# Kernel optimization log

Hardware: AMD Instinct MI355X
Metric: run time of the kernel (lower is better)

Reference implementation:

```python
import jax, jax.numpy as jnp
import numpy as np

B, Hs, Ws, DIM = 1, 48, 48, 768
NUM_HEADS, HEAD_DIM = 12, 64
RANK, ALPHA = 4, 1.0
SCALING = ALPHA / RANK
SCALE = HEAD_DIM ** -0.5


def setup_inputs() -> dict:
    key = jax.random.key(0)
    ks = jax.random.split(key, 13)
    s = lambda k, shape, sc=0.02: jax.random.normal(k, shape, jnp.float32) * sc
    return dict(
        x=jax.random.normal(ks[0], (B, Hs, Ws, DIM), jnp.float32),
        qkv_w=s(ks[1], (3 * DIM, DIM)),
        qkv_b=s(ks[2], (3 * DIM,)),
        proj_w=s(ks[3], (DIM, DIM)),
        proj_b=s(ks[4], (DIM,)),
        rel_pos_h=s(ks[5], (2 * Hs - 1, HEAD_DIM)),
        rel_pos_w=s(ks[6], (2 * Ws - 1, HEAD_DIM)),
        lora_q_A=s(ks[7], (RANK, DIM)),
        lora_q_B=s(ks[8], (DIM, RANK)),
        lora_k_A=s(ks[9], (RANK, DIM)),
        lora_k_B=s(ks[10], (DIM, RANK)),
        lora_v_A=s(ks[11], (RANK, DIM)),
        lora_v_B=s(ks[12], (DIM, RANK)),
    )


def _get_rel_pos(size, rel_pos):
    # q_size == k_size -> relative index = i - j + (size - 1)
    coords = jnp.arange(size)
    idx = coords[:, None] - coords[None, :] + (size - 1)
    return rel_pos[idx]  # [size, size, head_dim]


def reference(x, qkv_w, qkv_b, proj_w, proj_b, rel_pos_h, rel_pos_w,
              lora_q_A, lora_q_B, lora_k_A, lora_k_B, lora_v_A, lora_v_B):
    Bn, Hq, Wq, dim = x.shape
    N = Hq * Wq
    x_flat = x.reshape(Bn, N, dim)
    # frozen base qkv: [B, N, 3, nh, hd] -> [3, B, nh, N, hd]
    qkv = (x_flat @ qkv_w.T + qkv_b).reshape(Bn, N, 3, NUM_HEADS, HEAD_DIM)
    qkv = jnp.transpose(qkv, (2, 0, 3, 1, 4))

    def lora(A, Bm):
        d = (x_flat @ A.T @ Bm.T) * SCALING  # [B, N, dim]
        return jnp.transpose(d.reshape(Bn, N, NUM_HEADS, HEAD_DIM), (0, 2, 1, 3))

    q = (qkv[0] + lora(lora_q_A, lora_q_B)).reshape(Bn * NUM_HEADS, N, HEAD_DIM)
    k = (qkv[1] + lora(lora_k_A, lora_k_B)).reshape(Bn * NUM_HEADS, N, HEAD_DIM)
    v = (qkv[2] + lora(lora_v_A, lora_v_B)).reshape(Bn * NUM_HEADS, N, HEAD_DIM)

    attn = (q * SCALE) @ jnp.swapaxes(k, -2, -1)  # [B*nh, N, N]

    # decomposed relative position bias
    Rh = _get_rel_pos(Hq, rel_pos_h)  # [H, H, hd]
    Rw = _get_rel_pos(Wq, rel_pos_w)  # [W, W, hd]
    r_q = q.reshape(Bn * NUM_HEADS, Hq, Wq, HEAD_DIM)
    rel_h = jnp.einsum("bhwc,hkc->bhwk", r_q, Rh)
    rel_w = jnp.einsum("bhwc,wkc->bhwk", r_q, Rw)
    attn = (attn.reshape(-1, Hq, Wq, Hq, Wq)
            + rel_h[:, :, :, :, None]
            + rel_w[:, :, :, None, :]).reshape(-1, N, N)

    attn = jax.nn.softmax(attn, axis=-1)
    out = (attn @ v).reshape(Bn, NUM_HEADS, Hq, Wq, HEAD_DIM)
    out = jnp.transpose(out, (0, 2, 3, 1, 4)).reshape(Bn, Hq, Wq, dim)
    return out @ proj_w.T + proj_b
```

## Files before the change

### kernel.cpp

```cpp
#include <hip/hip_runtime.h>

#define NTOK 2304
#define NH 12
#define HD 64

typedef __attribute__((ext_vector_type(8))) short bf16x8;
typedef __attribute__((ext_vector_type(4))) float f32x4;

__device__ __forceinline__ unsigned short f2bf(float f){
  union { float f; unsigned u; } v; v.f = f;
  unsigned r = v.u + 0x7fffu + ((v.u >> 16) & 1u);
  return (unsigned short)(r >> 16);
}
__device__ __forceinline__ float bf2f(unsigned short h){
  union { unsigned u; float f; } v; v.u = ((unsigned)h) << 16;
  return v.f;
}
__device__ __forceinline__ float fast_exp2(float x){
  float r;
  asm("v_exp_f32 %0, %1" : "=v"(r) : "v"(x));
  return r;
}
__device__ __forceinline__ void gload_lds16(const void* g, void* lds){
  __builtin_amdgcn_global_load_lds(
    (const __attribute__((address_space(1))) unsigned int*)g,
    (__attribute__((address_space(3))) unsigned int*)lds, 16, 0, 0);
}

__global__ __launch_bounds__(256) void cvt_all(
    const float* __restrict__ x, const float* __restrict__ qw, const float* __restrict__ pw,
    unsigned short* __restrict__ xb, unsigned short* __restrict__ wqb, unsigned short* __restrict__ wpb){
  int i = blockIdx.x * 256 + threadIdx.x;
  const float* src; unsigned short* dst; int off;
  if (i < 442368)      { src = x;  dst = xb;  off = i; }
  else if (i < 884736) { src = qw; dst = wqb; off = i - 442368; }
  else                 { src = pw; dst = wpb; off = i - 884736; }
  float4 v = ((const float4*)src)[off];
  union { unsigned short u[4]; unsigned long long ll; } o;
  o.u[0] = f2bf(v.x); o.u[1] = f2bf(v.y); o.u[2] = f2bf(v.z); o.u[3] = f2bf(v.w);
  ((unsigned long long*)dst)[off] = o.ll;
}

__global__ __launch_bounds__(256) void lora_t_kernel(const float* __restrict__ x,
    const float* __restrict__ Aq, const float* __restrict__ Ak, const float* __restrict__ Av,
    float* __restrict__ t){
  int wave = (blockIdx.x * 256 + threadIdx.x) >> 6;
  int lane = threadIdx.x & 63;
  if (wave >= NTOK) return;
  const float* xr = x + (size_t)wave * 768;
  float part[12];
  #pragma unroll
  for (int j = 0; j < 12; j++) part[j] = 0.f;
  for (int k = lane; k < 768; k += 64){
    float xv = xr[k];
    #pragma unroll
    for (int r = 0; r < 4; r++){
      part[r]     += xv * Aq[r*768 + k];
      part[4 + r] += xv * Ak[r*768 + k];
      part[8 + r] += xv * Av[r*768 + k];
    }
  }
  #pragma unroll
  for (int j = 0; j < 12; j++){
    float v = part[j];
    #pragma unroll
    for (int off = 32; off; off >>= 1) v += __shfl_xor(v, off);
    if (lane == 0){
      int mat = j >> 2, r = j & 3;
      t[((size_t)mat * NTOK + wave) * 4 + r] = v;
    }
  }
}

__global__ __launch_bounds__(256) void qkv_gemm(
    const unsigned short* __restrict__ xg,
    const unsigned short* __restrict__ wg,
    const float* __restrict__ bias,
    const float* __restrict__ t,
    const float* __restrict__ Bq, const float* __restrict__ Bk, const float* __restrict__ Bv,
    unsigned short* __restrict__ qo,
    unsigned short* __restrict__ ko,
    unsigned short* __restrict__ vT)
{
  __shared__ short As[128*64];
  __shared__ short Bs[64*64];
  const int tid = threadIdx.x;
  const int lane = tid & 63;
  const int wv = tid >> 6;
  const int r = lane & 15, g = lane >> 4;
  const int wm = (wv >> 1) * 64, wn = (wv & 1) * 32;
  const int m0 = blockIdx.y * 128, n0 = blockIdx.x * 64;

  f32x4 acc[4][2];
  #pragma unroll
  for (int i = 0; i < 4; i++)
    #pragma unroll
    for (int j = 0; j < 2; j++) acc[i][j] = (f32x4){0.f, 0.f, 0.f, 0.f};

  for (int k0 = 0; k0 < 768; k0 += 64){
    __syncthreads();
    #pragma unroll
    for (int it = 0; it < 4; it++){
      int f = it * 256 + tid;
      int row = f >> 3, u = f & 7;
      int us = ((u ^ (row & 7)) << 3);
      gload_lds16(xg + (size_t)(m0 + row) * 768 + k0 + us, &As[f * 8]);
    }
    #pragma unroll
    for (int it = 0; it < 2; it++){
      int f = it * 256 + tid;
      int row = f >> 3, u = f & 7;
      int us = ((u ^ (row & 7)) << 3);
      gload_lds16(wg + (size_t)(n0 + row) * 768 + k0 + us, &Bs[f * 8]);
    }
    __syncthreads();
    #pragma unroll
    for (int ks = 0; ks < 2; ks++){
      bf16x8 af[4], bfr[2];
      #pragma unroll
      for (int mt = 0; mt < 4; mt++){
        int row = wm + mt * 16 + r;
        af[mt] = *(const bf16x8*)&As[row * 64 + ((((ks << 2) | g) ^ (r & 7)) << 3)];
      }
      #pragma unroll
      for (int nt = 0; nt < 2; nt++){
        int row = wn + nt * 16 + r;
        bfr[nt] = *(const bf16x8*)&Bs[row * 64 + ((((ks << 2) | g) ^ (r & 7)) << 3)];
      }
      #pragma unroll
      for (int mt = 0; mt < 4; mt++)
        #pragma unroll
        for (int nt = 0; nt < 2; nt++)
          acc[mt][nt] = __builtin_amdgcn_mfma_f32_16x16x32_bf16(af[mt], bfr[nt], acc[mt][nt], 0, 0, 0);
    }
  }

  const int part = n0 / 768;
  const float* Bl = (part == 0) ? Bq : ((part == 1) ? Bk : Bv);
  const float* tp = t + (size_t)part * NTOK * 4;
  #pragma unroll
  for (int mt = 0; mt < 4; mt++){
    #pragma unroll
    for (int reg = 0; reg < 4; reg++){
      int row_m = m0 + wm + mt * 16 + g * 4 + reg;
      float4 tv = *(const float4*)&tp[row_m * 4];
      #pragma unroll
      for (int nt = 0; nt < 2; nt++){
        int col = n0 + wn + nt * 16 + r;
        int cc = col - part * 768;
        float4 bw = *(const float4*)&Bl[cc * 4];
        float val = acc[mt][nt][reg] + bias[col]
                  + 0.25f * (tv.x * bw.x + tv.y * bw.y + tv.z * bw.z + tv.w * bw.w);
        int head = cc >> 6, d = cc & 63;
        if (part == 0)      qo[((size_t)head * NTOK + row_m) * 64 + d] = f2bf(val * 0.18033688f);
        else if (part == 1) ko[((size_t)head * NTOK + row_m) * 64 + d] = f2bf(val);
        else                vT[((size_t)head * 64 + d) * NTOK + row_m] = f2bf(val);
      }
    }
  }
}

__global__ __launch_bounds__(256, 2) void rel_gemm(
    const unsigned short* __restrict__ qg,
    const float* __restrict__ rph,
    const float* __restrict__ rpw,
    float* __restrict__ rel_h,
    float* __restrict__ rel_w)
{
  __shared__ float G[48 * 196];
  const int ih = blockIdx.x, head = blockIdx.y;
  const int tid = threadIdx.x, lane = tid & 63, wv = tid >> 6;
  const int r = lane & 15, g = lane >> 4;
  const int q0 = ih * 48;

  bf16x8 af[3][2];
  #pragma unroll
  for (int mt = 0; mt < 3; mt++)
    #pragma unroll
    for (int ks = 0; ks < 2; ks++)
      af[mt][ks] = *(const bf16x8*)&qg[((size_t)head * NTOK + q0 + mt * 16 + r) * 64 + ks * 32 + g * 8];

  bf16x8 bfv[3][2];
  #pragma unroll
  for (int nt = 0; nt < 3; nt++){
    int col = wv * 48 + nt * 16 + r;
    const float* src = (col < 95) ? &rph[(size_t)col * 64]
                     : (col < 190) ? &rpw[(size_t)(col - 95) * 64]
                     : &rpw[0];
    #pragma unroll
    for (int ks = 0; ks < 2; ks++){
      float4 lo = *(const float4*)&src[ks * 32 + g * 8];
      float4 hi = *(const float4*)&src[ks * 32 + g * 8 + 4];
      union { unsigned short u[8]; bf16x8 v; } t;
      t.u[0] = f2bf(lo.x); t.u[1] = f2bf(lo.y); t.u[2] = f2bf(lo.z); t.u[3] = f2bf(lo.w);
      t.u[4] = f2bf(hi.x); t.u[5] = f2bf(hi.y); t.u[6] = f2bf(hi.z); t.u[7] = f2bf(hi.w);
      bfv[nt][ks] = t.v;
    }
  }

  f32x4 acc[3][3];
  #pragma unroll
  for (int mt = 0; mt < 3; mt++)
    #pragma unroll
    for (int nt = 0; nt < 3; nt++) acc[mt][nt] = (f32x4){0.f, 0.f, 0.f, 0.f};
  #pragma unroll
  for (int ks = 0; ks < 2; ks++)
    #pragma unroll
    for (int mt = 0; mt < 3; mt++)
      #pragma unroll
      for (int nt = 0; nt < 3; nt++)
        acc[mt][nt] = __builtin_amdgcn_mfma_f32_16x16x32_bf16(af[mt][ks], bfv[nt][ks], acc[mt][nt], 0, 0, 0);

  #pragma unroll
  for (int mt = 0; mt < 3; mt++)
    #pragma unroll
    for (int reg = 0; reg < 4; reg++){
      int row = mt * 16 + g * 4 + reg;
      #pragma unroll
      for (int nt = 0; nt < 3; nt++)
        G[row * 196 + wv * 48 + nt * 16 + r] = acc[mt][nt][reg];
    }
  __syncthreads();

  for (int idx = tid; idx < 48 * 96; idx += 256){
    int i = idx / 96, c = idx % 96;
    size_t gi = (size_t)head * NTOK + q0 + i;
    if (c < 48) rel_h[gi * 48 + c]        = G[i * 196 + (ih + 47 - c)] * 8.f;
    else        rel_w[gi * 48 + (c - 48)] = G[i * 196 + 95 + (i + 47 - (c - 48))] * 8.f;
  }
}

__global__ __launch_bounds__(256, 3) void attn_kernel(
    const unsigned short* __restrict__ qg,
    const unsigned short* __restrict__ kg,
    const unsigned short* __restrict__ vT,
    const float* __restrict__ rel_h,
    const float* __restrict__ rel_w,
    unsigned short* __restrict__ ao)
{
  __shared__ __align__(16) char smem[46336];
  unsigned short* Ks = (unsigned short*)smem;
  unsigned short* Vs = (unsigned short*)(smem + 16384);
  float* relH = (float*)(smem + 32768);
  float* lsh = (float*)(smem + 46080);

  const int head = blockIdx.y;
  const int q0 = blockIdx.x * 64;
  const int tid = threadIdx.x, lane = tid & 63, wv = tid >> 6;
  const int r = lane & 15, g = lane >> 4;

  const unsigned short* kbase = kg + (size_t)head * NTOK * 64;
  const unsigned short* vbase = vT + (size_t)head * 64 * NTOK;

  for (int idx = tid; idx < 64 * 12; idx += 256){
    int i = idx / 12, c4 = idx % 12;
    *(float4*)&relH[i * 52 + c4 * 4] =
        *(const float4*)&rel_h[((size_t)head * NTOK + q0 + i) * 48 + c4 * 4];
  }

  float4 wreg[3];
  #pragma unroll
  for (int j = 0; j < 3; j++)
    wreg[j] = *(const float4*)&rel_w[((size_t)head * NTOK + q0 + wv * 16 + r) * 48 + j * 16 + g * 4];

  bf16x8 qf[2];
  #pragma unroll
  for (int ks = 0; ks < 2; ks++)
    qf[ks] = *(const bf16x8*)&qg[((size_t)head * NTOK + q0 + wv * 16 + r) * 64 + ks * 32 + g * 8];

  const int rowIn = lane >> 3, uu = lane & 7;

  #pragma unroll
  for (int s2 = 0; s2 < 2; s2++){
    int seg = wv * 2 + s2;
    int row = seg * 8 + rowIn;
    gload_lds16(kbase + (size_t)row * 64 + ((uu ^ (row & 7)) << 3), &Ks[seg * 512 + lane * 8]);
    gload_lds16(vbase + (size_t)row * NTOK + ((uu ^ (row & 7)) << 3), &Vs[seg * 512 + lane * 8]);
  }
  __syncthreads();

  f32x4 Oa[4];
  float lrun = 0.f;
  #pragma unroll
  for (int dt = 0; dt < 4; dt++) Oa[dt] = (f32x4){0.f, 0.f, 0.f, 0.f};

  const float* rsh = &relH[(wv * 16 + r) * 52];

  const int KH_T[3][4] = {{0,0,0,1},{1,1,2,2},{2,3,3,3}};
  const int J_T[3][4]  = {{0,1,2,0},{1,2,0,1},{2,0,1,2}};

  const int srcA = r + ((g & 1) << 5);
  const int srcB = srcA + 16;
  const int hi = (g >> 1);

  int buf = 0;
  for (int a = 0; a < 12; a++){
    #pragma unroll
    for (int tb = 0; tb < 3; tb++){
      const int t = a * 3 + tb;
      unsigned short* KsB = &Ks[buf * 4096];
      unsigned short* VsB = &Vs[buf * 4096];

      if (t < 35){
        const int key0n = (t + 1) * 64;
        unsigned short* KsN = &Ks[(buf ^ 1) * 4096];
        unsigned short* VsN = &Vs[(buf ^ 1) * 4096];
        #pragma unroll
        for (int s2 = 0; s2 < 2; s2++){
          int seg = wv * 2 + s2;
          int row = seg * 8 + rowIn;
          gload_lds16(kbase + (size_t)(key0n + row) * 64 + ((uu ^ (row & 7)) << 3),
                      &KsN[seg * 512 + lane * 8]);
          gload_lds16(vbase + (size_t)row * NTOK + key0n + ((uu ^ (row & 7)) << 3),
                      &VsN[seg * 512 + lane * 8]);
        }
      }

      f32x4 s[4];
      __builtin_amdgcn_s_setprio(1);
      #pragma unroll
      for (int ntl = 0; ntl < 4; ntl++){
        bf16x8 kc0 = *(const bf16x8*)&KsB[(ntl * 16 + r) * 64 + ((g ^ (r & 7)) << 3)];
        bf16x8 kc1 = *(const bf16x8*)&KsB[(ntl * 16 + r) * 64 + (((4 + g) ^ (r & 7)) << 3)];
        s[ntl] = (f32x4){0.f, 0.f, 0.f, 0.f};
        s[ntl] = __builtin_amdgcn_mfma_f32_16x16x32_bf16(kc0, qf[0], s[ntl], 0, 0, 0);
        s[ntl] = __builtin_amdgcn_mfma_f32_16x16x32_bf16(kc1, qf[1], s[ntl], 0, 0, 0);
      }
      __builtin_amdgcn_s_setprio(0);

      unsigned W0[4], W1[4];
      #pragma unroll
      for (int ntl = 0; ntl < 4; ntl++){
        float bh = rsh[4 * a + KH_T[tb][ntl]];
        float4 w = wreg[J_T[tb][ntl]];
        float p0 = fast_exp2(s[ntl][0] + bh + w.x);
        float p1 = fast_exp2(s[ntl][1] + bh + w.y);
        float p2 = fast_exp2(s[ntl][2] + bh + w.z);
        float p3 = fast_exp2(s[ntl][3] + bh + w.w);
        lrun += (p0 + p1) + (p2 + p3);
        asm("v_cvt_pk_bf16_f32 %0, %1, %2" : "=v"(W0[ntl]) : "v"(p0), "v"(p1));
        asm("v_cvt_pk_bf16_f32 %0, %1, %2" : "=v"(W1[ntl]) : "v"(p2), "v"(p3));
      }

      bf16x8 pf[2];
      #pragma unroll
      for (int ks = 0; ks < 2; ks++){
        unsigned a0 = (unsigned)__shfl((int)W0[2*ks],   srcA);
        unsigned a1 = (unsigned)__shfl((int)W0[2*ks+1], srcA);
        unsigned b0 = (unsigned)__shfl((int)W1[2*ks],   srcA);
        unsigned b1 = (unsigned)__shfl((int)W1[2*ks+1], srcA);
        unsigned c0 = (unsigned)__shfl((int)W0[2*ks],   srcB);
        unsigned c1 = (unsigned)__shfl((int)W0[2*ks+1], srcB);
        unsigned d0 = (unsigned)__shfl((int)W1[2*ks],   srcB);
        unsigned d1 = (unsigned)__shfl((int)W1[2*ks+1], srcB);
        union { unsigned w[4]; bf16x8 v; } u;
        u.w[0] = hi ? a1 : a0;
        u.w[1] = hi ? b1 : b0;
        u.w[2] = hi ? c1 : c0;
        u.w[3] = hi ? d1 : d0;
        pf[ks] = u.v;
      }

      __builtin_amdgcn_s_setprio(1);
      #pragma unroll
      for (int dt = 0; dt < 4; dt++){
        #pragma unroll
        for (int ks = 0; ks < 2; ks++){
          bf16x8 vf = *(const bf16x8*)&VsB[(dt * 16 + r) * 64 + (((ks * 4 + g) ^ (r & 7)) << 3)];
          Oa[dt] = __builtin_amdgcn_mfma_f32_16x16x32_bf16(pf[ks], vf, Oa[dt], 0, 0, 0);
        }
      }
      __builtin_amdgcn_s_setprio(0);

      __syncthreads();
      buf ^= 1;
    }
  }

  {
    float l = lrun;
    l += __shfl_xor(l, 16);
    l += __shfl_xor(l, 32);
    if (lane < 16) lsh[wv * 16 + lane] = l;
  }
  __syncthreads();
  float invL[4];
  #pragma unroll
  for (int reg = 0; reg < 4; reg++) invL[reg] = 1.f / lsh[wv * 16 + g * 4 + reg];
  #pragma unroll
  for (int dt = 0; dt < 4; dt++)
    #pragma unroll
    for (int reg = 0; reg < 4; reg++){
      int token = q0 + wv * 16 + g * 4 + reg;
      ao[(size_t)token * 768 + head * 64 + dt * 16 + r] = f2bf(Oa[dt][reg] * invL[reg]);
    }
}

__global__ __launch_bounds__(256) void proj_gemm(
    const unsigned short* __restrict__ ag,
    const unsigned short* __restrict__ wg,
    const float* __restrict__ bias,
    float* __restrict__ out)
{
  __shared__ short As[64*64];
  __shared__ short Bs[64*64];
  const int tid = threadIdx.x;
  const int lane = tid & 63;
  const int wv = tid >> 6;
  const int r = lane & 15, g = lane >> 4;
  const int wm = (wv >> 1) * 32, wn = (wv & 1) * 32;
  const int m0 = blockIdx.y * 64, n0 = blockIdx.x * 64;

  f32x4 acc[2][2];
  #pragma unroll
  for (int i = 0; i < 2; i++)
    #pragma unroll
    for (int j = 0; j < 2; j++) acc[i][j] = (f32x4){0.f, 0.f, 0.f, 0.f};

  for (int k0 = 0; k0 < 768; k0 += 64){
    __syncthreads();
    #pragma unroll
    for (int it = 0; it < 2; it++){
      int f = it * 256 + tid;
      int row = f >> 3, u = f & 7;
      int us = ((u ^ (row & 7)) << 3);
      gload_lds16(ag + (size_t)(m0 + row) * 768 + k0 + us, &As[f * 8]);
      gload_lds16(wg + (size_t)(n0 + row) * 768 + k0 + us, &Bs[f * 8]);
    }
    __syncthreads();
    #pragma unroll
    for (int ks = 0; ks < 2; ks++){
      bf16x8 af[2], bfr[2];
      #pragma unroll
      for (int mt = 0; mt < 2; mt++){
        int row = wm + mt * 16 + r;
        af[mt] = *(const bf16x8*)&As[row * 64 + ((((ks << 2) | g) ^ (r & 7)) << 3)];
      }
      #pragma unroll
      for (int nt = 0; nt < 2; nt++){
        int row = wn + nt * 16 + r;
        bfr[nt] = *(const bf16x8*)&Bs[row * 64 + ((((ks << 2) | g) ^ (r & 7)) << 3)];
      }
      #pragma unroll
      for (int mt = 0; mt < 2; mt++)
        #pragma unroll
        for (int nt = 0; nt < 2; nt++)
          acc[mt][nt] = __builtin_amdgcn_mfma_f32_16x16x32_bf16(af[mt], bfr[nt], acc[mt][nt], 0, 0, 0);
    }
  }

  #pragma unroll
  for (int mt = 0; mt < 2; mt++)
    #pragma unroll
    for (int reg = 0; reg < 4; reg++){
      int row_m = m0 + wm + mt * 16 + g * 4 + reg;
      #pragma unroll
      for (int nt = 0; nt < 2; nt++){
        int col = n0 + wn + nt * 16 + r;
        out[(size_t)row_m * 768 + col] = acc[mt][nt][reg] + bias[col];
      }
    }
}

extern "C" void kernel_launch(void* const* d_in, const int* in_sizes, int n_in,
                              void* d_out, int out_size, void* d_ws, size_t ws_size,
                              hipStream_t stream){
  (void)in_sizes; (void)n_in; (void)out_size; (void)ws_size;
  const float* x      = (const float*)d_in[0];
  const float* qkv_w  = (const float*)d_in[1];
  const float* qkv_b  = (const float*)d_in[2];
  const float* proj_w = (const float*)d_in[3];
  const float* proj_b = (const float*)d_in[4];
  const float* rph    = (const float*)d_in[5];
  const float* rpw    = (const float*)d_in[6];
  const float* Aq     = (const float*)d_in[7];
  const float* Bq     = (const float*)d_in[8];
  const float* Ak     = (const float*)d_in[9];
  const float* Bk     = (const float*)d_in[10];
  const float* Av     = (const float*)d_in[11];
  const float* Bv     = (const float*)d_in[12];

  char* w = (char*)d_ws;
  unsigned short* xb  = (unsigned short*)(w + 0);
  unsigned short* wqb = (unsigned short*)(w + 3538944);
  unsigned short* wpb = (unsigned short*)(w + 7077888);
  unsigned short* qb  = (unsigned short*)(w + 8257536);
  unsigned short* kb  = (unsigned short*)(w + 11796480);
  unsigned short* vtb = (unsigned short*)(w + 15335424);
  float* tb           = (float*)(w + 18874368);
  float* rhb          = (float*)(w + 18984960);
  float* rwb          = (float*)(w + 24293376);
  unsigned short* aob = (unsigned short*)(w + 29601792);

  cvt_all<<<4032, 256, 0, stream>>>(x, qkv_w, proj_w, xb, wqb, wpb);
  lora_t_kernel<<<576, 256, 0, stream>>>(x, Aq, Ak, Av, tb);
  qkv_gemm<<<dim3(36, 18), 256, 0, stream>>>(xb, wqb, qkv_b, tb, Bq, Bk, Bv, qb, kb, vtb);
  rel_gemm<<<dim3(48, 12), 256, 0, stream>>>(qb, rph, rpw, rhb, rwb);
  attn_kernel<<<dim3(36, 12), 256, 0, stream>>>(qb, kb, vtb, rhb, rwb, aob);
  proj_gemm<<<dim3(12, 36), 256, 0, stream>>>(aob, wpb, proj_b, (float*)d_out);
}
```

Measured before the change: 109.6 us.

## Double key tile to 128 per iteration in attention kernel

```diff
diff --git a/kernel.cpp b/kernel.cpp
--- a/kernel.cpp
+++ b/kernel.cpp
@@ -230,7 +230,7 @@
   }
 }
 
-__global__ __launch_bounds__(256, 3) void attn_kernel(
+__global__ __launch_bounds__(256, 2) void attn_kernel(
     const unsigned short* __restrict__ qg,
     const unsigned short* __restrict__ kg,
     const unsigned short* __restrict__ vT,
@@ -238,11 +238,11 @@
     const float* __restrict__ rel_w,
     unsigned short* __restrict__ ao)
 {
-  __shared__ __align__(16) char smem[46336];
+  __shared__ __align__(16) char smem[79104];
   unsigned short* Ks = (unsigned short*)smem;
-  unsigned short* Vs = (unsigned short*)(smem + 16384);
-  float* relH = (float*)(smem + 32768);
-  float* lsh = (float*)(smem + 46080);
+  unsigned short* Vs = (unsigned short*)(smem + 32768);
+  float* relH = (float*)(smem + 65536);
+  float* lsh = (float*)(smem + 78848);
 
   const int head = blockIdx.y;
   const int q0 = blockIdx.x * 64;
@@ -268,15 +268,27 @@
   for (int ks = 0; ks < 2; ks++)
     qf[ks] = *(const bf16x8*)&qg[((size_t)head * NTOK + q0 + wv * 16 + r) * 64 + ks * 32 + g * 8];
 
-  const int rowIn = lane >> 3, uu = lane & 7;
-
-  #pragma unroll
-  for (int s2 = 0; s2 < 2; s2++){
-    int seg = wv * 2 + s2;
-    int row = seg * 8 + rowIn;
-    gload_lds16(kbase + (size_t)row * 64 + ((uu ^ (row & 7)) << 3), &Ks[seg * 512 + lane * 8]);
-    gload_lds16(vbase + (size_t)row * NTOK + ((uu ^ (row & 7)) << 3), &Vs[seg * 512 + lane * 8]);
-  }
+  const int rowIn  = lane >> 3, uu  = lane & 7;
+  const int rowIn4 = lane >> 4, u16 = lane & 15;
+
+#define STAGE_TILE(T, BUFP) do { \
+    const int key0_ = (T) * 128; \
+    unsigned short* KsX = &Ks[(BUFP) * 8192]; \
+    unsigned short* VsX = &Vs[(BUFP) * 8192]; \
+    _Pragma("unroll") \
+    for (int s2 = 0; s2 < 4; s2++){ \
+      int segk = wv * 4 + s2; \
+      int rowk = segk * 8 + rowIn; \
+      gload_lds16(kbase + (size_t)(key0_ + rowk) * 64 + ((uu ^ (rowk & 7)) << 3), \
+                  &KsX[segk * 512 + lane * 8]); \
+      int segv = wv * 4 + s2; \
+      int rowv = segv * 4 + rowIn4; \
+      gload_lds16(vbase + (size_t)rowv * NTOK + key0_ + ((u16 ^ (rowv & 7)) << 3), \
+                  &VsX[segv * 512 + lane * 8]); \
+    } \
+  } while(0)
+
+  STAGE_TILE(0, 0);
   __syncthreads();
 
   f32x4 Oa[4];
@@ -286,40 +298,27 @@
 
   const float* rsh = &relH[(wv * 16 + r) * 52];
 
-  const int KH_T[3][4] = {{0,0,0,1},{1,1,2,2},{2,3,3,3}};
-  const int J_T[3][4]  = {{0,1,2,0},{1,2,0,1},{2,0,1,2}};
+  const int KH8[3][8] = {{0,0,0,1,1,1,2,2},{2,3,3,3,4,4,4,5},{5,5,6,6,6,7,7,7}};
+  const int J8[3][8]  = {{0,1,2,0,1,2,0,1},{2,0,1,2,0,1,2,0},{1,2,0,1,2,0,1,2}};
 
   const int srcA = r + ((g & 1) << 5);
   const int srcB = srcA + 16;
   const int hi = (g >> 1);
 
   int buf = 0;
-  for (int a = 0; a < 12; a++){
+  for (int a = 0; a < 6; a++){
     #pragma unroll
     for (int tb = 0; tb < 3; tb++){
       const int t = a * 3 + tb;
-      unsigned short* KsB = &Ks[buf * 4096];
-      unsigned short* VsB = &Vs[buf * 4096];
-
-      if (t < 35){
-        const int key0n = (t + 1) * 64;
-        unsigned short* KsN = &Ks[(buf ^ 1) * 4096];
-        unsigned short* VsN = &Vs[(buf ^ 1) * 4096];
-        #pragma unroll
-        for (int s2 = 0; s2 < 2; s2++){
-          int seg = wv * 2 + s2;
-          int row = seg * 8 + rowIn;
-          gload_lds16(kbase + (size_t)(key0n + row) * 64 + ((uu ^ (row & 7)) << 3),
-                      &KsN[seg * 512 + lane * 8]);
-          gload_lds16(vbase + (size_t)row * NTOK + key0n + ((uu ^ (row & 7)) << 3),
-                      &VsN[seg * 512 + lane * 8]);
-        }
-      }
-
-      f32x4 s[4];
+      unsigned short* KsB = &Ks[buf * 8192];
+      unsigned short* VsB = &Vs[buf * 8192];
+
+      if (t < 17) STAGE_TILE(t + 1, buf ^ 1);
+
+      f32x4 s[8];
       __builtin_amdgcn_s_setprio(1);
       #pragma unroll
-      for (int ntl = 0; ntl < 4; ntl++){
+      for (int ntl = 0; ntl < 8; ntl++){
         bf16x8 kc0 = *(const bf16x8*)&KsB[(ntl * 16 + r) * 64 + ((g ^ (r & 7)) << 3)];
         bf16x8 kc1 = *(const bf16x8*)&KsB[(ntl * 16 + r) * 64 + (((4 + g) ^ (r & 7)) << 3)];
         s[ntl] = (f32x4){0.f, 0.f, 0.f, 0.f};
@@ -328,11 +327,11 @@
       }
       __builtin_amdgcn_s_setprio(0);
 
-      unsigned W0[4], W1[4];
-      #pragma unroll
-      for (int ntl = 0; ntl < 4; ntl++){
-        float bh = rsh[4 * a + KH_T[tb][ntl]];
-        float4 w = wreg[J_T[tb][ntl]];
+      unsigned W0[8], W1[8];
+      #pragma unroll
+      for (int ntl = 0; ntl < 8; ntl++){
+        float bh = rsh[8 * a + KH8[tb][ntl]];
+        float4 w = wreg[J8[tb][ntl]];
         float p0 = fast_exp2(s[ntl][0] + bh + w.x);
         float p1 = fast_exp2(s[ntl][1] + bh + w.y);
         float p2 = fast_exp2(s[ntl][2] + bh + w.z);
@@ -342,9 +341,9 @@
         asm("v_cvt_pk_bf16_f32 %0, %1, %2" : "=v"(W1[ntl]) : "v"(p2), "v"(p3));
       }
 
-      bf16x8 pf[2];
-      #pragma unroll
-      for (int ks = 0; ks < 2; ks++){
+      bf16x8 pf[4];
+      #pragma unroll
+      for (int ks = 0; ks < 4; ks++){
         unsigned a0 = (unsigned)__shfl((int)W0[2*ks],   srcA);
         unsigned a1 = (unsigned)__shfl((int)W0[2*ks+1], srcA);
         unsigned b0 = (unsigned)__shfl((int)W1[2*ks],   srcA);
@@ -365,8 +364,8 @@
       #pragma unroll
       for (int dt = 0; dt < 4; dt++){
         #pragma unroll
-        for (int ks = 0; ks < 2; ks++){
-          bf16x8 vf = *(const bf16x8*)&VsB[(dt * 16 + r) * 64 + (((ks * 4 + g) ^ (r & 7)) << 3)];
+        for (int ks = 0; ks < 4; ks++){
+          bf16x8 vf = *(const bf16x8*)&VsB[(dt * 16 + r) * 128 + (((ks * 4 + g) ^ (r & 7)) << 3)];
           Oa[dt] = __builtin_amdgcn_mfma_f32_16x16x32_bf16(pf[ks], vf, Oa[dt], 0, 0, 0);
         }
       }
@@ -376,6 +375,7 @@
       buf ^= 1;
     }
   }
+#undef STAGE_TILE
 
   {
     float l = lrun;
```

New measurement: 110.6 us. Within noise of the previous version (+0.9%).
